# Optimization experiments

Hardware: AMD Instinct MI355X
Metric: run time of the kernel (lower is better)

## Reference

```python
import jax, jax.numpy as jnp
import numpy as np

EPS = 1e-5

def _conv1d(x, w, b):
    # x: [N, Cin, L], w: [Cout, Cin, 3], SAME padding (pad=1)
    y = jax.lax.conv_general_dilated(
        x, w, window_strides=(1,), padding=((1, 1),),
        dimension_numbers=("NCH", "OIH", "NCH"))
    return y + b[None, :, None]

def _bn(x, gamma, beta, mean, var):
    # inference-mode BatchNorm1d over channel dim
    inv = gamma / jnp.sqrt(var + EPS)
    return x * inv[None, :, None] + (beta - mean * inv)[None, :, None]

def _make_params(key):
    ks = jax.random.split(key, 9)
    def w(k, o, i):
        return jax.random.normal(k, (o, i, 3), jnp.float32) * (1.0 / np.sqrt(i * 3))
    p = {}
    p["w1"], p["b1"] = w(ks[0], 128, 1), jnp.zeros((128,), jnp.float32)
    p["w2"], p["b2"] = w(ks[1], 256, 128), jnp.zeros((256,), jnp.float32)
    p["w3"], p["b3"] = w(ks[2], 256, 256), jnp.zeros((256,), jnp.float32)
    for i, c in zip((1, 2, 3), (128, 256, 256)):
        p[f"g{i}"] = jnp.ones((c,), jnp.float32)
        p[f"be{i}"] = jnp.zeros((c,), jnp.float32)
        p[f"m{i}"] = jax.random.normal(ks[2 + i], (c,), jnp.float32) * 0.1
        p[f"v{i}"] = 1.0 + 0.1 * jax.random.uniform(ks[5 + i], (c,), jnp.float32)
    return p

def setup_inputs() -> dict:
    key = jax.random.key(0)
    kx, kp = jax.random.split(key)
    inp = {"x": jax.random.normal(kx, (16, 64, 520), jnp.float32)}
    inp.update(_make_params(kp))
    return inp

def reference(x, w1, b1, w2, b2, w3, b3,
              g1, be1, m1, v1, g2, be2, m2, v2, g3, be3, m3, v3):
    B, T, D = x.shape
    h = x.reshape(B * T, 1, D)                     # fuse time into batch
    h = jax.nn.relu(_bn(_conv1d(h, w1, b1), g1, be1, m1, v1))
    h = jax.nn.relu(_bn(_conv1d(h, w2, b2), g2, be2, m2, v2))
    h = jax.nn.relu(_bn(_conv1d(h, w3, b3), g3, be3, m3, v3))
    out = h.mean(axis=-1)                          # AdaptiveAvgPool1d(1) + squeeze
    return out.reshape(B, T, -1)                   # [B, T, feature_dim]
```

## Files before the change

kernel.cpp:

```cpp
#include <hip/hip_runtime.h>
#include <hip/hip_bf16.h>

#define EPSV 1e-5f

typedef __attribute__((ext_vector_type(8))) short short8;
typedef __attribute__((ext_vector_type(4))) short short4v;
typedef __attribute__((ext_vector_type(4))) float f32x4;

static __device__ __forceinline__ short f2bf(float f) {
    unsigned int u = __builtin_bit_cast(unsigned int, f);
    unsigned int r = (u + 0x7FFFu + ((u >> 16) & 1u)) >> 16;
    return (short)(r & 0xFFFFu);
}
static __device__ __forceinline__ f32x4 zero4() { f32x4 z = {0.f, 0.f, 0.f, 0.f}; return z; }

static __device__ __forceinline__ void gload16(const void* g, void* l) {
    __builtin_amdgcn_global_load_lds((const unsigned int*)g, (unsigned int*)l, 16, 0, 0);
}

__global__ void sfe_prep(
    const float* __restrict__ w1, const float* __restrict__ b1,
    const float* __restrict__ w2, const float* __restrict__ b2,
    const float* __restrict__ w3, const float* __restrict__ b3,
    const float* __restrict__ g1, const float* __restrict__ be1,
    const float* __restrict__ m1, const float* __restrict__ v1,
    const float* __restrict__ g2, const float* __restrict__ be2,
    const float* __restrict__ m2, const float* __restrict__ v2,
    const float* __restrict__ g3, const float* __restrict__ be3,
    const float* __restrict__ m3, const float* __restrict__ v3,
    short* __restrict__ W2f, short* __restrict__ W3f,
    float* __restrict__ s1o, float* __restrict__ bb1o,
    float* __restrict__ bb2o, float* __restrict__ bb3o)
{
    int idx = blockIdx.x * 256 + threadIdx.x;
    int e = idx & 7, lane = (idx >> 3) & 63, ct = (idx >> 9) & 15;
    int lr = lane & 15, lg = lane >> 4;
    {
        int kc = idx >> 13;
        int c3 = ct * 16 + lr;
        int c2in = (kc & 7) * 32 + lg * 8 + e;
        int dk = kc >> 3;
        float s = g3[c3] / sqrtf(v3[c3] + EPSV);
        W3f[idx] = f2bf(w3[(c3 * 256 + c2in) * 3 + dk] * s);
    }
    if (idx < 98304) {
        int kc = idx >> 13;
        int c2 = ct * 16 + lr;
        int ci = (kc & 3) * 32 + lg * 8 + e;
        int dk = kc >> 2;
        float s = g2[c2] / sqrtf(v2[c2] + EPSV);
        W2f[idx] = f2bf(w2[(c2 * 128 + ci) * 3 + dk] * s);
    }
    if (idx < 128) {
        float s = g1[idx] / sqrtf(v1[idx] + EPSV);
        s1o[idx]  = s;
        bb1o[idx] = (b1[idx] - m1[idx]) * s + be1[idx];
    }
    if (idx < 256) {
        float s2 = g2[idx] / sqrtf(v2[idx] + EPSV);
        bb2o[idx] = (b2[idx] - m2[idx]) * s2 + be2[idx];
        float s3 = g3[idx] / sqrtf(v3[idx] + EPSV);
        bb3o[idx] = (b3[idx] - m3[idx]) * s3 + be3[idx];
    }
}

#define MFMA16(A, B, C) __builtin_amdgcn_mfma_f32_16x16x32_bf16(A, B, C, 0, 0, 0)

__global__ __launch_bounds__(512, 1) void sfe_l12(
    const float* __restrict__ x, const float* __restrict__ w1,
    const short* __restrict__ W2f,
    const float* __restrict__ s1a, const float* __restrict__ bb1a,
    const float* __restrict__ bb2a,
    char* __restrict__ h2g, int seq0)
{
    __shared__ __align__(16) char ring[32768];
    __shared__ __align__(16) char obuf[2][16384];
    __shared__ float xs[528];

    const int tid = threadIdx.x, lane = tid & 63, wid = tid >> 6;
    const int lr = lane & 15, lg = lane >> 4;
    const int seq = seq0 + blockIdx.x;
    char* h2b = h2g + (size_t)blockIdx.x * 270336;

    const int c4 = (tid & 31) * 4;
    float w1r[12];
    #pragma unroll
    for (int e2 = 0; e2 < 4; ++e2) {
        w1r[e2 * 3 + 0] = w1[(c4 + e2) * 3 + 0];
        w1r[e2 * 3 + 1] = w1[(c4 + e2) * 3 + 1];
        w1r[e2 * 3 + 2] = w1[(c4 + e2) * 3 + 2];
    }
    const f32x4 s1v = *reinterpret_cast<const f32x4*>(s1a + c4);
    const f32x4 b1v = *reinterpret_cast<const f32x4*>(bb1a + c4);

    short8 W2r[24];
    #pragma unroll
    for (int kc = 0; kc < 12; ++kc) {
        #pragma unroll
        for (int p = 0; p < 2; ++p)
            W2r[kc * 2 + p] = *reinterpret_cast<const short8*>(
                W2f + ((kc * 16 + wid * 2 + p) * 64 + lane) * 8);
    }
    const f32x4 bias0 = *reinterpret_cast<const f32x4*>(bb2a + (wid * 2 + 0) * 16 + lg * 4);
    const f32x4 bias1 = *reinterpret_cast<const f32x4*>(bb2a + (wid * 2 + 1) * 16 + lg * 4);

    for (int i = tid; i < 528; i += 512) {
        int l = i - 1;
        xs[i] = (l >= 0 && l < 520) ? x[(size_t)seq * 520 + l] : 0.f;
    }
    *reinterpret_cast<long long*>(ring + 28672 + tid * 8) = 0ll;
    __syncthreads();

    auto h1chunk = [&](int X) {
        int row = X * 16 + (tid >> 5);
        int rr = (row + 128) & 127;
        short4v hv;
        if (row < 520) {
            float x0 = xs[row], x1 = xs[row + 1], x2 = xs[row + 2];
            #pragma unroll
            for (int e2 = 0; e2 < 4; ++e2) {
                float a = w1r[e2 * 3] * x0 + w1r[e2 * 3 + 1] * x1 + w1r[e2 * 3 + 2] * x2;
                hv[e2] = f2bf(fmaxf(a * s1v[e2] + b1v[e2], 0.f));
            }
        } else {
            hv[0] = 0; hv[1] = 0; hv[2] = 0; hv[3] = 0;
        }
        int ch = c4 >> 3;
        *reinterpret_cast<short4v*>(
            ring + rr * 256 + ((ch ^ (row & 15)) << 4) + (c4 & 7) * 2) = hv;
    };

    h1chunk(0); h1chunk(1); h1chunk(2);
    __syncthreads();

    auto epi = [&](const f32x4& A, int p, const f32x4& bv, int jt, int b) {
        int c2b = (wid * 2 + p) * 16 + lg * 4;
        int ch = c2b >> 3;
        short4v hv;
        #pragma unroll
        for (int r = 0; r < 4; ++r) hv[r] = f2bf(fmaxf(A[r] + bv[r], 0.f));
        *reinterpret_cast<short4v*>(
            obuf[b] + (jt * 16 + lr) * 512 + ((ch ^ lr) << 4) + (c2b & 7) * 2) = hv;
    };

    for (int C = 0; C <= 32; C += 2) {
        const bool do2 = (C < 32);
        const int b = (C >> 1) & 1;
        f32x4 a00 = zero4(), a10 = zero4(), a01 = zero4(), a11 = zero4();
        const int row0base = C * 16 + lr - 1;

        if (do2) {
            #pragma unroll
            for (int kc = 0; kc < 12; ++kc) {
                int dk = kc >> 2, cc = kc & 3;
                int ch = cc * 4 + lg;
                int row0 = row0base + dk, row1 = row0 + 16;
                short8 B0 = *reinterpret_cast<const short8*>(
                    ring + ((row0 + 128) & 127) * 256 + ((ch ^ (row0 & 15)) << 4));
                short8 B1 = *reinterpret_cast<const short8*>(
                    ring + ((row1 + 128) & 127) * 256 + ((ch ^ (row1 & 15)) << 4));
                a00 = MFMA16(W2r[kc * 2 + 0], B0, a00);
                a10 = MFMA16(W2r[kc * 2 + 1], B0, a10);
                a01 = MFMA16(W2r[kc * 2 + 0], B1, a01);
                a11 = MFMA16(W2r[kc * 2 + 1], B1, a11);
            }
        } else {
            #pragma unroll
            for (int kc = 0; kc < 12; ++kc) {
                int dk = kc >> 2, cc = kc & 3;
                int ch = cc * 4 + lg;
                int row0 = row0base + dk;
                short8 B0 = *reinterpret_cast<const short8*>(
                    ring + ((row0 + 128) & 127) * 256 + ((ch ^ (row0 & 15)) << 4));
                a00 = MFMA16(W2r[kc * 2 + 0], B0, a00);
                a10 = MFMA16(W2r[kc * 2 + 1], B0, a10);
            }
        }

        if (C + 3 <= 32) h1chunk(C + 3);
        if (C + 4 <= 32) h1chunk(C + 4);

        epi(a00, 0, bias0, 0, b);
        epi(a10, 1, bias1, 0, b);
        if (do2) { epi(a01, 0, bias0, 1, b); epi(a11, 1, bias1, 1, b); }

        asm volatile("s_waitcnt lgkmcnt(0)" ::: "memory");
        __builtin_amdgcn_s_barrier();

        #pragma unroll
        for (int q = 0; q < 2; ++q) {
            int byteo = q * 8192 + tid * 16;
            int lrow = byteo >> 9;
            int grow = C * 16 + lrow;
            if (grow < 528 && (do2 || lrow < 16)) {
                short8 d = *reinterpret_cast<const short8*>(obuf[b] + byteo);
                if (grow >= 520) { short8 z = {0,0,0,0,0,0,0,0}; d = z; }
                *reinterpret_cast<short8*>(h2b + (size_t)grow * 512 + (byteo & 511)) = d;
            }
        }
    }
}

__global__ __launch_bounds__(256, 1) void sfe_l3(
    const char* __restrict__ h2g, const short* __restrict__ W3f,
    const float* __restrict__ bb3a, float* __restrict__ out, int seq0)
{
    __shared__ __align__(16) char ring[65536];

    const int tid = threadIdx.x, lane = tid & 63, wid = tid >> 6;
    const int lr = lane & 15, lg = lane >> 4;
    const int bi = blockIdx.x;
    const int seq = seq0 + (bi >> 1);
    const int ch2 = bi & 1;
    const char* h2b = h2g + (size_t)(bi >> 1) * 270336;

    short8 W3r[48];
    #pragma unroll
    for (int kc = 0; kc < 24; ++kc) {
        #pragma unroll
        for (int p = 0; p < 2; ++p)
            W3r[kc * 2 + p] = *reinterpret_cast<const short8*>(
                W3f + ((kc * 16 + ch2 * 8 + wid * 2 + p) * 64 + lane) * 8);
    }
    const f32x4 bias0 = *reinterpret_cast<const f32x4*>(bb3a + (ch2 * 8 + wid * 2 + 0) * 16 + lg * 4);
    const f32x4 bias1 = *reinterpret_cast<const f32x4*>(bb3a + (ch2 * 8 + wid * 2 + 1) * 16 + lg * 4);
    f32x4 pool0 = zero4(), pool1 = zero4();

    auto stage = [&](int X) {
        int Xc = X > 32 ? 32 : X;
        #pragma unroll
        for (int q = 0; q < 2; ++q)
            gload16(h2b + Xc * 8192 + q * 4096 + tid * 16,
                    ring + (X & 7) * 8192 + q * 4096 + tid * 16);
    };

    #pragma unroll
    for (int q = 0; q < 2; ++q)
        *reinterpret_cast<f32x4*>(ring + 57344 + q * 4096 + tid * 16) = zero4();
    stage(0); stage(1); stage(2); stage(3); stage(4);
    asm volatile("s_waitcnt vmcnt(4) lgkmcnt(0)" ::: "memory");
    __builtin_amdgcn_s_barrier();

    for (int C = 0; C <= 32; C += 2) {
        stage(C + 5); stage(C + 6);
        __builtin_amdgcn_sched_barrier(0);

        const bool do2 = (C < 32);
        f32x4 a00 = zero4(), a10 = zero4(), a01 = zero4(), a11 = zero4();
        const int row0base = C * 16 + lr - 1;

        auto readB = [&](int kc, int jt) -> short8 {
            int dk = kc >> 3, cc = kc & 7;
            int ch = cc * 4 + lg;
            int row = row0base + dk + jt * 16;
            return *reinterpret_cast<const short8*>(
                ring + ((row + 128) & 127) * 512 + ((ch ^ (row & 15)) << 4));
        };
        auto mfma4 = [&](int kc, const short8& B0, const short8& B1) {
            a00 = MFMA16(W3r[kc * 2 + 0], B0, a00);
            a10 = MFMA16(W3r[kc * 2 + 1], B0, a10);
            a01 = MFMA16(W3r[kc * 2 + 0], B1, a01);
            a11 = MFMA16(W3r[kc * 2 + 1], B1, a11);
        };

        if (do2) {
            short8 B0a[8], B1a[8], B0b[8], B1b[8];
            #pragma unroll
            for (int k = 0; k < 8; ++k) { B0a[k] = readB(k, 0); B1a[k] = readB(k, 1); }
            __builtin_amdgcn_sched_barrier(0);
            #pragma unroll
            for (int k = 0; k < 8; ++k) { B0b[k] = readB(k + 8, 0); B1b[k] = readB(k + 8, 1); }
            __builtin_amdgcn_sched_barrier(0);
            #pragma unroll
            for (int k = 0; k < 8; ++k) mfma4(k, B0a[k], B1a[k]);
            __builtin_amdgcn_sched_barrier(0);
            #pragma unroll
            for (int k = 0; k < 8; ++k) { B0a[k] = readB(k + 16, 0); B1a[k] = readB(k + 16, 1); }
            __builtin_amdgcn_sched_barrier(0);
            #pragma unroll
            for (int k = 0; k < 8; ++k) mfma4(k + 8, B0b[k], B1b[k]);
            #pragma unroll
            for (int k = 0; k < 8; ++k) mfma4(k + 16, B0a[k], B1a[k]);
        } else {
            short8 B0a[12], B0b[12];
            #pragma unroll
            for (int k = 0; k < 12; ++k) B0a[k] = readB(k, 0);
            __builtin_amdgcn_sched_barrier(0);
            #pragma unroll
            for (int k = 0; k < 12; ++k) B0b[k] = readB(k + 12, 0);
            __builtin_amdgcn_sched_barrier(0);
            #pragma unroll
            for (int k = 0; k < 12; ++k) {
                a00 = MFMA16(W3r[k * 2 + 0], B0a[k], a00);
                a10 = MFMA16(W3r[k * 2 + 1], B0a[k], a10);
            }
            #pragma unroll
            for (int k = 0; k < 12; ++k) {
                a00 = MFMA16(W3r[(k + 12) * 2 + 0], B0b[k], a00);
                a10 = MFMA16(W3r[(k + 12) * 2 + 1], B0b[k], a10);
            }
        }

        {
            bool v0 = (C * 16 + lr) < 520;
            f32x4 t0, t1;
            #pragma unroll
            for (int r = 0; r < 4; ++r) {
                t0[r] = fmaxf(a00[r] + bias0[r], 0.f);
                t1[r] = fmaxf(a10[r] + bias1[r], 0.f);
            }
            pool0 += v0 ? t0 : zero4();
            pool1 += v0 ? t1 : zero4();
            if (do2) {
                #pragma unroll
                for (int r = 0; r < 4; ++r) {
                    t0[r] = fmaxf(a01[r] + bias0[r], 0.f);
                    t1[r] = fmaxf(a11[r] + bias1[r], 0.f);
                }
                pool0 += t0;
                pool1 += t1;
            }
        }

        asm volatile("s_waitcnt vmcnt(4) lgkmcnt(0)" ::: "memory");
        __builtin_amdgcn_s_barrier();
    }

    asm volatile("s_waitcnt vmcnt(0)" ::: "memory");

    #pragma unroll
    for (int d = 1; d < 16; d <<= 1) {
        #pragma unroll
        for (int r = 0; r < 4; ++r) {
            pool0[r] += __shfl_xor(pool0[r], d, 64);
            pool1[r] += __shfl_xor(pool1[r], d, 64);
        }
    }
    if (lr == 0) {
        f32x4 o0, o1;
        #pragma unroll
        for (int r = 0; r < 4; ++r) { o0[r] = pool0[r] * (1.f / 520.f); o1[r] = pool1[r] * (1.f / 520.f); }
        *reinterpret_cast<f32x4*>(out + (size_t)seq * 256 + (ch2 * 8 + wid * 2 + 0) * 16 + lg * 4) = o0;
        *reinterpret_cast<f32x4*>(out + (size_t)seq * 256 + (ch2 * 8 + wid * 2 + 1) * 16 + lg * 4) = o1;
    }
}

extern "C" void kernel_launch(void* const* d_in, const int* in_sizes, int n_in,
                              void* d_out, int out_size, void* d_ws, size_t ws_size,
                              hipStream_t stream) {
    (void)n_in; (void)out_size;
    const float* x   = (const float*)d_in[0];
    const float* w1  = (const float*)d_in[1];
    const float* b1  = (const float*)d_in[2];
    const float* w2  = (const float*)d_in[3];
    const float* b2  = (const float*)d_in[4];
    const float* w3  = (const float*)d_in[5];
    const float* b3  = (const float*)d_in[6];
    const float* g1  = (const float*)d_in[7];
    const float* be1 = (const float*)d_in[8];
    const float* m1  = (const float*)d_in[9];
    const float* v1  = (const float*)d_in[10];
    const float* g2  = (const float*)d_in[11];
    const float* be2 = (const float*)d_in[12];
    const float* m2  = (const float*)d_in[13];
    const float* v2  = (const float*)d_in[14];
    const float* g3  = (const float*)d_in[15];
    const float* be3 = (const float*)d_in[16];
    const float* m3  = (const float*)d_in[17];
    const float* v3  = (const float*)d_in[18];

    char* ws = (char*)d_ws;
    short* W2f  = (short*)(ws);
    short* W3f  = (short*)(ws + 196608);
    float* s1o  = (float*)(ws + 589824);
    float* bb1o = (float*)(ws + 590336);
    float* bb2o = (float*)(ws + 590848);
    float* bb3o = (float*)(ws + 591872);
    char*  h2g  = ws + (1 << 20);

    int nseq = in_sizes[0] / 520;
    size_t h2cap = ws_size > (size_t)(1 << 20) ? ws_size - (1 << 20) : 0;
    int maxseq = (int)(h2cap / 270336);
    if (maxseq < 1) maxseq = 1;
    if (maxseq > nseq) maxseq = nseq;

    sfe_prep<<<768, 256, 0, stream>>>(w1, b1, w2, b2, w3, b3,
                                      g1, be1, m1, v1, g2, be2, m2, v2,
                                      g3, be3, m3, v3,
                                      W2f, W3f, s1o, bb1o, bb2o, bb3o);
    for (int s0 = 0; s0 < nseq; s0 += maxseq) {
        int n = (nseq - s0) < maxseq ? (nseq - s0) : maxseq;
        sfe_l12<<<n, 512, 0, stream>>>(x, w1, W2f, s1o, bb1o, bb2o, h2g, s0);
        sfe_l3 <<<n * 2, 256, 0, stream>>>(h2g, W3f, bb3o, (float*)d_out, s0);
    }
}
```

Measured before the change: 440.3 us.

## Split layer-2 conv across two blocks per sequence by output-channel half

Layer 1+2 now launches two 256-thread blocks per sequence, each computing half of the 256 layer-2 output channels, with the output staging buffer halved and writes offset by channel half. Layer 1 is recomputed redundantly in both blocks. The B-operand LDS reads are also batched ahead of the MFMAs with sched_barriers to hide LDS latency. This is meant to raise occupancy and parallelism across CUs at the cost of duplicated layer-1 work and more register pressure from the prefetched operands.

After: 522.7 us. +18.7%, slower.

```diff
diff --git a/kernel.cpp b/kernel.cpp
--- a/kernel.cpp
+++ b/kernel.cpp
@@ -66,7 +66,7 @@
 
 #define MFMA16(A, B, C) __builtin_amdgcn_mfma_f32_16x16x32_bf16(A, B, C, 0, 0, 0)
 
-__global__ __launch_bounds__(512, 1) void sfe_l12(
+__global__ __launch_bounds__(256, 1) void sfe_l12(
     const float* __restrict__ x, const float* __restrict__ w1,
     const short* __restrict__ W2f,
     const float* __restrict__ s1a, const float* __restrict__ bb1a,
@@ -74,15 +74,18 @@
     char* __restrict__ h2g, int seq0)
 {
     __shared__ __align__(16) char ring[32768];
-    __shared__ __align__(16) char obuf[2][16384];
+    __shared__ __align__(16) char obuf[2][8192];
     __shared__ float xs[528];
 
     const int tid = threadIdx.x, lane = tid & 63, wid = tid >> 6;
     const int lr = lane & 15, lg = lane >> 4;
-    const int seq = seq0 + blockIdx.x;
-    char* h2b = h2g + (size_t)blockIdx.x * 270336;
+    const int bi = blockIdx.x;
+    const int seq = seq0 + (bi >> 1);
+    const int ch2 = bi & 1;
+    char* h2b = h2g + (size_t)(bi >> 1) * 270336;
 
     const int c4 = (tid & 31) * 4;
+    const int chw = c4 >> 3;
     float w1r[12];
     #pragma unroll
     for (int e2 = 0; e2 < 4; ++e2) {
@@ -99,48 +102,51 @@
         #pragma unroll
         for (int p = 0; p < 2; ++p)
             W2r[kc * 2 + p] = *reinterpret_cast<const short8*>(
-                W2f + ((kc * 16 + wid * 2 + p) * 64 + lane) * 8);
-    }
-    const f32x4 bias0 = *reinterpret_cast<const f32x4*>(bb2a + (wid * 2 + 0) * 16 + lg * 4);
-    const f32x4 bias1 = *reinterpret_cast<const f32x4*>(bb2a + (wid * 2 + 1) * 16 + lg * 4);
-
-    for (int i = tid; i < 528; i += 512) {
+                W2f + ((kc * 16 + ch2 * 8 + wid * 2 + p) * 64 + lane) * 8);
+    }
+    const f32x4 bias0 = *reinterpret_cast<const f32x4*>(bb2a + (ch2 * 8 + wid * 2 + 0) * 16 + lg * 4);
+    const f32x4 bias1 = *reinterpret_cast<const f32x4*>(bb2a + (ch2 * 8 + wid * 2 + 1) * 16 + lg * 4);
+
+    for (int i = tid; i < 528; i += 256) {
         int l = i - 1;
         xs[i] = (l >= 0 && l < 520) ? x[(size_t)seq * 520 + l] : 0.f;
     }
-    *reinterpret_cast<long long*>(ring + 28672 + tid * 8) = 0ll;
+    *reinterpret_cast<f32x4*>(ring + 28672 + tid * 16) = zero4();
     __syncthreads();
 
     auto h1chunk = [&](int X) {
-        int row = X * 16 + (tid >> 5);
-        int rr = (row + 128) & 127;
-        short4v hv;
-        if (row < 520) {
-            float x0 = xs[row], x1 = xs[row + 1], x2 = xs[row + 2];
-            #pragma unroll
-            for (int e2 = 0; e2 < 4; ++e2) {
-                float a = w1r[e2 * 3] * x0 + w1r[e2 * 3 + 1] * x1 + w1r[e2 * 3 + 2] * x2;
-                hv[e2] = f2bf(fmaxf(a * s1v[e2] + b1v[e2], 0.f));
-            }
-        } else {
-            hv[0] = 0; hv[1] = 0; hv[2] = 0; hv[3] = 0;
-        }
-        int ch = c4 >> 3;
-        *reinterpret_cast<short4v*>(
-            ring + rr * 256 + ((ch ^ (row & 15)) << 4) + (c4 & 7) * 2) = hv;
+        #pragma unroll
+        for (int rh = 0; rh < 2; ++rh) {
+            int row = X * 16 + rh * 8 + (tid >> 5);
+            int rr = row & 127;
+            short4v hv;
+            if (row < 520) {
+                float x0 = xs[row], x1 = xs[row + 1], x2 = xs[row + 2];
+                #pragma unroll
+                for (int e2 = 0; e2 < 4; ++e2) {
+                    float a = w1r[e2 * 3] * x0 + w1r[e2 * 3 + 1] * x1 + w1r[e2 * 3 + 2] * x2;
+                    hv[e2] = f2bf(fmaxf(a * s1v[e2] + b1v[e2], 0.f));
+                }
+            } else {
+                hv[0] = 0; hv[1] = 0; hv[2] = 0; hv[3] = 0;
+            }
+            *reinterpret_cast<short4v*>(
+                ring + rr * 256 + ((chw ^ (row & 15)) << 4) + (c4 & 7) * 2) = hv;
+        }
     };
 
     h1chunk(0); h1chunk(1); h1chunk(2);
     __syncthreads();
 
     auto epi = [&](const f32x4& A, int p, const f32x4& bv, int jt, int b) {
-        int c2b = (wid * 2 + p) * 16 + lg * 4;
-        int ch = c2b >> 3;
+        int c2b = (ch2 * 8 + wid * 2 + p) * 16 + lg * 4;
+        int chl = c2b & 127;
+        int chv = chl >> 3;
         short4v hv;
         #pragma unroll
         for (int r = 0; r < 4; ++r) hv[r] = f2bf(fmaxf(A[r] + bv[r], 0.f));
         *reinterpret_cast<short4v*>(
-            obuf[b] + (jt * 16 + lr) * 512 + ((ch ^ lr) << 4) + (c2b & 7) * 2) = hv;
+            obuf[b] + (jt * 16 + lr) * 256 + ((chv ^ lr) << 4) + (chl & 7) * 2) = hv;
     };
 
     for (int C = 0; C <= 32; C += 2) {
@@ -149,31 +155,49 @@
         f32x4 a00 = zero4(), a10 = zero4(), a01 = zero4(), a11 = zero4();
         const int row0base = C * 16 + lr - 1;
 
+        auto readB = [&](int kc, int jt) -> short8 {
+            int dk = kc >> 2, cc = kc & 3;
+            int ch = cc * 4 + lg;
+            int row = row0base + dk + jt * 16;
+            return *reinterpret_cast<const short8*>(
+                ring + ((row + 128) & 127) * 256 + ((ch ^ (row & 15)) << 4));
+        };
+        auto mfma4 = [&](int kc, const short8& B0, const short8& B1) {
+            a00 = MFMA16(W2r[kc * 2 + 0], B0, a00);
+            a10 = MFMA16(W2r[kc * 2 + 1], B0, a10);
+            a01 = MFMA16(W2r[kc * 2 + 0], B1, a01);
+            a11 = MFMA16(W2r[kc * 2 + 1], B1, a11);
+        };
+
         if (do2) {
-            #pragma unroll
-            for (int kc = 0; kc < 12; ++kc) {
-                int dk = kc >> 2, cc = kc & 3;
-                int ch = cc * 4 + lg;
-                int row0 = row0base + dk, row1 = row0 + 16;
-                short8 B0 = *reinterpret_cast<const short8*>(
-                    ring + ((row0 + 128) & 127) * 256 + ((ch ^ (row0 & 15)) << 4));
-                short8 B1 = *reinterpret_cast<const short8*>(
-                    ring + ((row1 + 128) & 127) * 256 + ((ch ^ (row1 & 15)) << 4));
-                a00 = MFMA16(W2r[kc * 2 + 0], B0, a00);
-                a10 = MFMA16(W2r[kc * 2 + 1], B0, a10);
-                a01 = MFMA16(W2r[kc * 2 + 0], B1, a01);
-                a11 = MFMA16(W2r[kc * 2 + 1], B1, a11);
-            }
+            short8 B0a[6], B1a[6], B0b[6], B1b[6];
+            #pragma unroll
+            for (int k = 0; k < 6; ++k) { B0a[k] = readB(k, 0); B1a[k] = readB(k, 1); }
+            __builtin_amdgcn_sched_barrier(0);
+            #pragma unroll
+            for (int k = 0; k < 6; ++k) { B0b[k] = readB(k + 6, 0); B1b[k] = readB(k + 6, 1); }
+            __builtin_amdgcn_sched_barrier(0);
+            #pragma unroll
+            for (int k = 0; k < 6; ++k) mfma4(k, B0a[k], B1a[k]);
+            #pragma unroll
+            for (int k = 0; k < 6; ++k) mfma4(k + 6, B0b[k], B1b[k]);
         } else {
-            #pragma unroll
-            for (int kc = 0; kc < 12; ++kc) {
-                int dk = kc >> 2, cc = kc & 3;
-                int ch = cc * 4 + lg;
-                int row0 = row0base + dk;
-                short8 B0 = *reinterpret_cast<const short8*>(
-                    ring + ((row0 + 128) & 127) * 256 + ((ch ^ (row0 & 15)) << 4));
-                a00 = MFMA16(W2r[kc * 2 + 0], B0, a00);
-                a10 = MFMA16(W2r[kc * 2 + 1], B0, a10);
+            short8 B0a[6], B0b[6];
+            #pragma unroll
+            for (int k = 0; k < 6; ++k) B0a[k] = readB(k, 0);
+            __builtin_amdgcn_sched_barrier(0);
+            #pragma unroll
+            for (int k = 0; k < 6; ++k) B0b[k] = readB(k + 6, 0);
+            __builtin_amdgcn_sched_barrier(0);
+            #pragma unroll
+            for (int k = 0; k < 6; ++k) {
+                a00 = MFMA16(W2r[k * 2 + 0], B0a[k], a00);
+                a10 = MFMA16(W2r[k * 2 + 1], B0a[k], a10);
+            }
+            #pragma unroll
+            for (int k = 0; k < 6; ++k) {
+                a00 = MFMA16(W2r[(k + 6) * 2 + 0], B0b[k], a00);
+                a10 = MFMA16(W2r[(k + 6) * 2 + 1], B0b[k], a10);
             }
         }
 
@@ -189,13 +213,14 @@
 
         #pragma unroll
         for (int q = 0; q < 2; ++q) {
-            int byteo = q * 8192 + tid * 16;
-            int lrow = byteo >> 9;
+            int byteo = q * 4096 + tid * 16;
+            int lrow = byteo >> 8;
             int grow = C * 16 + lrow;
             if (grow < 528 && (do2 || lrow < 16)) {
                 short8 d = *reinterpret_cast<const short8*>(obuf[b] + byteo);
                 if (grow >= 520) { short8 z = {0,0,0,0,0,0,0,0}; d = z; }
-                *reinterpret_cast<short8*>(h2b + (size_t)grow * 512 + (byteo & 511)) = d;
+                *reinterpret_cast<short8*>(
+                    h2b + (size_t)grow * 512 + ch2 * 256 + (byteo & 255)) = d;
             }
         }
     }
@@ -390,7 +415,7 @@
                                       W2f, W3f, s1o, bb1o, bb2o, bb3o);
     for (int s0 = 0; s0 < nseq; s0 += maxseq) {
         int n = (nseq - s0) < maxseq ? (nseq - s0) : maxseq;
-        sfe_l12<<<n, 512, 0, stream>>>(x, w1, W2f, s1o, bb1o, bb2o, h2g, s0);
+        sfe_l12<<<n * 2, 256, 0, stream>>>(x, w1, W2f, s1o, bb1o, bb2o, h2g, s0);
         sfe_l3 <<<n * 2, 256, 0, stream>>>(h2g, W3f, bb3o, (float*)d_out, s0);
     }
 }
```

## Widen layer-3 tile to four row-tiles with a deeper LDS ring and precomputed offsets

Applied to the files above, without the earlier changes.

The layer-3 conv kernel now processes four 16-row tiles per iteration instead of two. It grows the LDS ring from 8 to 12 slots (96KB) and stages four chunks ahead, with a software-pipelined double-buffered issue/consume schedule of LDS reads and MFMAs. Swizzled column offsets are precomputed once, and the final partial tile is peeled into a separate tail block. The aim is fewer barriers per row processed and more MFMA work per LDS round trip. In exchange it uses more registers for the B fragments and accumulators and much more LDS, which could add register pressure and spills.

Measured after the change: 427.2 us, median of 2. 1.03x faster.

```diff
diff --git a/kernel.cpp b/kernel.cpp
--- a/kernel.cpp
+++ b/kernel.cpp
@@ -205,7 +205,7 @@
     const char* __restrict__ h2g, const short* __restrict__ W3f,
     const float* __restrict__ bb3a, float* __restrict__ out, int seq0)
 {
-    __shared__ __align__(16) char ring[65536];
+    __shared__ __align__(16) char ring[98304];
 
     const int tid = threadIdx.x, lane = tid & 63, wid = tid >> 6;
     const int lr = lane & 15, lg = lane >> 4;
@@ -226,104 +226,132 @@
     const f32x4 bias1 = *reinterpret_cast<const f32x4*>(bb3a + (ch2 * 8 + wid * 2 + 1) * 16 + lg * 4);
     f32x4 pool0 = zero4(), pool1 = zero4();
 
+    int Koff[24];
+    #pragma unroll
+    for (int kc = 0; kc < 24; ++kc) {
+        int dk = kc >> 3, cc = kc & 7;
+        Koff[kc] = (((cc * 4 + lg) ^ ((lr - 1 + dk) & 15)) << 4);
+    }
+
     auto stage = [&](int X) {
         int Xc = X > 32 ? 32 : X;
+        int slot = X % 12;
         #pragma unroll
         for (int q = 0; q < 2; ++q)
             gload16(h2b + Xc * 8192 + q * 4096 + tid * 16,
-                    ring + (X & 7) * 8192 + q * 4096 + tid * 16);
+                    ring + slot * 8192 + q * 4096 + tid * 16);
     };
 
     #pragma unroll
     for (int q = 0; q < 2; ++q)
-        *reinterpret_cast<f32x4*>(ring + 57344 + q * 4096 + tid * 16) = zero4();
-    stage(0); stage(1); stage(2); stage(3); stage(4);
+        *reinterpret_cast<f32x4*>(ring + 90112 + q * 4096 + tid * 16) = zero4();
+    stage(0); stage(1); stage(2); stage(3); stage(4); stage(5); stage(6);
     asm volatile("s_waitcnt vmcnt(4) lgkmcnt(0)" ::: "memory");
     __builtin_amdgcn_s_barrier();
 
-    for (int C = 0; C <= 32; C += 2) {
-        stage(C + 5); stage(C + 6);
+    #define RD(rbarr, KC, JT) \
+        (*reinterpret_cast<const short8*>(ring + rbarr[(JT) * 3 + ((KC) >> 3)] + Koff[(KC)]))
+
+    for (int S = 0; S <= 28; S += 4) {
+        stage(S + 7); stage(S + 8); stage(S + 9); stage(S + 10);
         __builtin_amdgcn_sched_barrier(0);
 
-        const bool do2 = (C < 32);
-        f32x4 a00 = zero4(), a10 = zero4(), a01 = zero4(), a11 = zero4();
-        const int row0base = C * 16 + lr - 1;
-
-        auto readB = [&](int kc, int jt) -> short8 {
-            int dk = kc >> 3, cc = kc & 7;
-            int ch = cc * 4 + lg;
-            int row = row0base + dk + jt * 16;
-            return *reinterpret_cast<const short8*>(
-                ring + ((row + 128) & 127) * 512 + ((ch ^ (row & 15)) << 4));
-        };
-        auto mfma4 = [&](int kc, const short8& B0, const short8& B1) {
-            a00 = MFMA16(W3r[kc * 2 + 0], B0, a00);
-            a10 = MFMA16(W3r[kc * 2 + 1], B0, a10);
-            a01 = MFMA16(W3r[kc * 2 + 0], B1, a01);
-            a11 = MFMA16(W3r[kc * 2 + 1], B1, a11);
-        };
-
-        if (do2) {
-            short8 B0a[8], B1a[8], B0b[8], B1b[8];
+        int rb[12];
+        #pragma unroll
+        for (int jt = 0; jt < 4; ++jt) {
             #pragma unroll
-            for (int k = 0; k < 8; ++k) { B0a[k] = readB(k, 0); B1a[k] = readB(k, 1); }
+            for (int dk = 0; dk < 3; ++dk)
+                rb[jt * 3 + dk] = (((S + jt) * 16 + lr - 1 + dk + 192) % 192) * 512;
+        }
+
+        f32x4 a0[4] = {zero4(), zero4(), zero4(), zero4()};
+        f32x4 a1[4] = {zero4(), zero4(), zero4(), zero4()};
+        short8 Ba[16], Bb[16];
+
+        #define ISSUE(BUF, KCB) \
+            _Pragma("unroll") for (int k = 0; k < 4; ++k) { \
+                _Pragma("unroll") for (int jt = 0; jt < 4; ++jt) \
+                    BUF[k * 4 + jt] = RD(rb, (KCB) + k, jt); \
+            } \
             __builtin_amdgcn_sched_barrier(0);
-            #pragma unroll
-            for (int k = 0; k < 8; ++k) { B0b[k] = readB(k + 8, 0); B1b[k] = readB(k + 8, 1); }
+
+        #define CONSUME(BUF, KCB) \
+            _Pragma("unroll") for (int k = 0; k < 4; ++k) { \
+                _Pragma("unroll") for (int jt = 0; jt < 4; ++jt) { \
+                    a0[jt] = MFMA16(W3r[((KCB) + k) * 2 + 0], BUF[k * 4 + jt], a0[jt]); \
+                    a1[jt] = MFMA16(W3r[((KCB) + k) * 2 + 1], BUF[k * 4 + jt], a1[jt]); \
+                } \
+            } \
             __builtin_amdgcn_sched_barrier(0);
-            #pragma unroll
-            for (int k = 0; k < 8; ++k) mfma4(k, B0a[k], B1a[k]);
-            __builtin_amdgcn_sched_barrier(0);
-            #pragma unroll
-            for (int k = 0; k < 8; ++k) { B0a[k] = readB(k + 16, 0); B1a[k] = readB(k + 16, 1); }
-            __builtin_amdgcn_sched_barrier(0);
-            #pragma unroll
-            for (int k = 0; k < 8; ++k) mfma4(k + 8, B0b[k], B1b[k]);
-            #pragma unroll
-            for (int k = 0; k < 8; ++k) mfma4(k + 16, B0a[k], B1a[k]);
-        } else {
-            short8 B0a[12], B0b[12];
-            #pragma unroll
-            for (int k = 0; k < 12; ++k) B0a[k] = readB(k, 0);
-            __builtin_amdgcn_sched_barrier(0);
-            #pragma unroll
-            for (int k = 0; k < 12; ++k) B0b[k] = readB(k + 12, 0);
-            __builtin_amdgcn_sched_barrier(0);
-            #pragma unroll
-            for (int k = 0; k < 12; ++k) {
-                a00 = MFMA16(W3r[k * 2 + 0], B0a[k], a00);
-                a10 = MFMA16(W3r[k * 2 + 1], B0a[k], a10);
-            }
-            #pragma unroll
-            for (int k = 0; k < 12; ++k) {
-                a00 = MFMA16(W3r[(k + 12) * 2 + 0], B0b[k], a00);
-                a10 = MFMA16(W3r[(k + 12) * 2 + 1], B0b[k], a10);
-            }
-        }
-
-        {
-            bool v0 = (C * 16 + lr) < 520;
+
+        ISSUE(Ba, 0)
+        ISSUE(Bb, 4)
+        CONSUME(Ba, 0)
+        ISSUE(Ba, 8)
+        CONSUME(Bb, 4)
+        ISSUE(Bb, 12)
+        CONSUME(Ba, 8)
+        ISSUE(Ba, 16)
+        CONSUME(Bb, 12)
+        ISSUE(Bb, 20)
+        CONSUME(Ba, 16)
+        CONSUME(Bb, 20)
+
+        #undef ISSUE
+        #undef CONSUME
+
+        #pragma unroll
+        for (int jt = 0; jt < 4; ++jt) {
             f32x4 t0, t1;
             #pragma unroll
             for (int r = 0; r < 4; ++r) {
-                t0[r] = fmaxf(a00[r] + bias0[r], 0.f);
-                t1[r] = fmaxf(a10[r] + bias1[r], 0.f);
+                t0[r] = fmaxf(a0[jt][r] + bias0[r], 0.f);
+                t1[r] = fmaxf(a1[jt][r] + bias1[r], 0.f);
             }
-            pool0 += v0 ? t0 : zero4();
-            pool1 += v0 ? t1 : zero4();
-            if (do2) {
-                #pragma unroll
-                for (int r = 0; r < 4; ++r) {
-                    t0[r] = fmaxf(a01[r] + bias0[r], 0.f);
-                    t1[r] = fmaxf(a11[r] + bias1[r], 0.f);
-                }
-                pool0 += t0;
-                pool1 += t1;
-            }
+            pool0 += t0;
+            pool1 += t1;
         }
 
         asm volatile("s_waitcnt vmcnt(4) lgkmcnt(0)" ::: "memory");
         __builtin_amdgcn_s_barrier();
+    }
+
+    {
+        int rbT[3];
+        #pragma unroll
+        for (int dk = 0; dk < 3; ++dk)
+            rbT[dk] = ((512 + lr - 1 + dk + 192) % 192) * 512;
+
+        f32x4 a00 = zero4(), a10 = zero4();
+        short8 Ta[12], Tb[12];
+        #pragma unroll
+        for (int k = 0; k < 12; ++k)
+            Ta[k] = *reinterpret_cast<const short8*>(ring + rbT[k >> 3] + Koff[k]);
+        __builtin_amdgcn_sched_barrier(0);
+        #pragma unroll
+        for (int k = 0; k < 12; ++k)
+            Tb[k] = *reinterpret_cast<const short8*>(ring + rbT[(k + 12) >> 3] + Koff[k + 12]);
+        __builtin_amdgcn_sched_barrier(0);
+        #pragma unroll
+        for (int k = 0; k < 12; ++k) {
+            a00 = MFMA16(W3r[k * 2 + 0], Ta[k], a00);
+            a10 = MFMA16(W3r[k * 2 + 1], Ta[k], a10);
+        }
+        #pragma unroll
+        for (int k = 0; k < 12; ++k) {
+            a00 = MFMA16(W3r[(k + 12) * 2 + 0], Tb[k], a00);
+            a10 = MFMA16(W3r[(k + 12) * 2 + 1], Tb[k], a10);
+        }
+
+        bool v0 = (512 + lr) < 520;
+        f32x4 t0, t1;
+        #pragma unroll
+        for (int r = 0; r < 4; ++r) {
+            t0[r] = fmaxf(a00[r] + bias0[r], 0.f);
+            t1[r] = fmaxf(a10[r] + bias1[r], 0.f);
+        }
+        pool0 += v0 ? t0 : zero4();
+        pool1 += v0 ? t1 : zero4();
     }
 
     asm volatile("s_waitcnt vmcnt(0)" ::: "memory");
```
